# Optimization experiments

Hardware: AMD Instinct MI355X
Metric: run time of the kernel (lower is better)

The kernel has to match this reference:

```python
import jax, jax.numpy as jnp
import numpy as np

E = 8        # n_routed_experts
K = 4        # num_experts_per_tok
T = 1024     # tokens
H = 1024     # hidden_size
I = 1408     # moe_intermediate_size


def setup_inputs() -> dict:
    key = jax.random.key(0)
    ks = jax.random.split(key, 6)
    hidden_states = jax.random.normal(ks[0], (T, H), jnp.float32)
    rw = jax.random.uniform(ks[1], (T, K), jnp.float32)
    router_weights = rw / jnp.sum(rw, axis=-1, keepdims=True)  # normalized top-k router weights
    selected_experts = jax.random.randint(ks[2], (T, K), 0, E, jnp.int32)
    gate_w = jax.random.normal(ks[3], (E, H, I), jnp.float32) * (H ** -0.5)  # lecun_normal-ish
    up_w = jax.random.normal(ks[4], (E, H, I), jnp.float32) * (H ** -0.5)
    down_w = jax.random.normal(ks[5], (E, I, H), jnp.float32) * (I ** -0.5)
    return {
        'hidden_states': hidden_states,
        'router_weights': router_weights,
        'gate_w': gate_w,
        'up_w': up_w,
        'down_w': down_w,
        'selected_experts': selected_experts,
    }


def _grouped_matmul(x, w, seg):
    # x: [m, k] tokens sorted by expert; w: [E, k, n]; seg: [m] expert id per row.
    # Grouped GEMM expressed as E masked GEMMs (fixed small loop over experts);
    # a custom kernel would do true variable-group-size grouped GEMM.
    out = jnp.zeros((x.shape[0], w.shape[-1]), x.dtype)
    for e in range(w.shape[0]):
        out = out + jnp.where((seg == e)[:, None], x, jnp.zeros((), x.dtype)) @ w[e]
    return out


def reference(hidden_states, router_weights, gate_w, up_w, down_w, selected_experts):
    t, k = selected_experts.shape
    flat = selected_experts.ravel()                       # [t*k]
    hs = jnp.repeat(hidden_states, k, axis=0)             # [t*k, H]
    sort_idx = jnp.argsort(flat)                          # dispatch: sort tokens by expert
    seg = flat[sort_idx]
    xs = hs[sort_idx]
    gate = _grouped_matmul(xs, gate_w, seg)               # [t*k, I]
    up = _grouped_matmul(xs, up_w, seg)                   # [t*k, I]
    h = jax.nn.silu(gate) * up                            # fused SwiGLU
    down = _grouped_matmul(h, down_w, seg)                # [t*k, H]
    unsort = jnp.argsort(sort_idx)                        # scatter back to token order
    out = down[unsort].reshape(t, k, -1)
    return jnp.sum(out * router_weights[..., None], axis=1)  # weighted combine [t, H]
```

## Files before the change

### kernel.cpp

```cpp
#include <hip/hip_runtime.h>
#include <hip/hip_bf16.h>
#include <cstdint>
#include <cstddef>

#define NE 8
#define NT 1024
#define NK 4
#define NH 1024
#define NI 1408
#define NA (NT * NK)
#define BM 128
#define MAXTILES 40
#define PADSLOTS 5120

typedef short short8 __attribute__((ext_vector_type(8)));
typedef float f32x4 __attribute__((ext_vector_type(4)));
typedef float f4v __attribute__((ext_vector_type(4)));
typedef unsigned short u16;

#define WS_HDR   0
#define WS_SORT  1024
#define WS_XBF   21504
#define WS_GT    2118656
#define WS_UT    25187328
#define WS_DT    48256000
#define WS_HB    71324672

__device__ __forceinline__ u16 f2b(float f) {
  union { float f; uint32_t u; } c; c.f = f;
  uint32_t u = c.u;
  return (u16)((u + 0x7FFFu + ((u >> 16) & 1u)) >> 16);
}

__device__ __forceinline__ void llds16(const void* g, void* l) {
  __builtin_amdgcn_global_load_lds(
      (const __attribute__((address_space(1))) void*)g,
      (__attribute__((address_space(3))) void*)l, 16, 0, 0);
}

__device__ __forceinline__ void transcvt_stripe(const float* __restrict__ src,
                                                u16* __restrict__ dst,
                                                int K, int N, int k0, int n0,
                                                u16* smem, int tid) {
  u16 (*t2)[64][64] = (u16(*)[64][64])smem;
  int r = tid >> 4, c = tid & 15;
  f4v v[2][4];
#pragma unroll
  for (int t = 0; t < 2; ++t)
#pragma unroll
    for (int i = 0; i < 4; ++i)
      v[t][i] = __builtin_nontemporal_load(
          (const f4v*)&src[(size_t)(k0 + r + 16 * i) * N + n0 + t * 64 + c * 4]);
#pragma unroll
  for (int t = 0; t < 2; ++t)
#pragma unroll
    for (int i = 0; i < 4; ++i) {
      ushort4 o;
      o.x = f2b(v[t][i].x); o.y = f2b(v[t][i].y); o.z = f2b(v[t][i].z); o.w = f2b(v[t][i].w);
      int row = r + 16 * i;
      int sc = (c * 4) ^ (row & 56);
      *(ushort4*)&t2[t][row][sc] = o;
    }
  __syncthreads();
#pragma unroll
  for (int t = 0; t < 2; ++t)
#pragma unroll
    for (int i = 0; i < 2; ++i) {
      int idx = i * 256 + tid;
      int n = idx >> 3, kc = idx & 7;
      int cs = n ^ (kc * 8);
      u16 o[8];
#pragma unroll
      for (int j = 0; j < 8; ++j) o[j] = t2[t][kc * 8 + j][cs];
      *(short8*)&dst[(size_t)(n0 + t * 64 + n) * K + k0 + kc * 8] = *(const short8*)o;
    }
}

__global__ __launch_bounds__(256) void k1_prep(
    const float* __restrict__ gw, const float* __restrict__ uw, const float* __restrict__ dw,
    const float* __restrict__ hs, const int* __restrict__ sel,
    u16* __restrict__ gT, u16* __restrict__ uT, u16* __restrict__ dT, u16* __restrict__ xbf,
    int* __restrict__ hdr, int* __restrict__ sorted, float* __restrict__ outz) {
  int tid = threadIdx.x;
  int y = blockIdx.y;
  if (y == 24) {
    for (int i = blockIdx.x * 256 + tid; i * 4 < NT * NH; i += 176 * 256) {
      f4v v = __builtin_nontemporal_load((const f4v*)&hs[i * 4]);
      ushort4 o;
      o.x = f2b(v.x); o.y = f2b(v.y); o.z = f2b(v.z); o.w = f2b(v.w);
      *(ushort4*)&xbf[i * 4] = o;
    }
    return;
  }
  if (y == 25) {
    int x = blockIdx.x;
    if (x >= 1 && x <= 64) {
      int base = (x - 1) * 16384;
      f4v z = {0.f, 0.f, 0.f, 0.f};
#pragma unroll
      for (int i = 0; i < 16; ++i)
        *(f4v*)&outz[base + (i * 256 + tid) * 4] = z;
      return;
    }
    if (x != 0) return;
    __shared__ int cnt[NE], fill[NE], poff_s[NE + 1];
    if (tid < NE) { cnt[tid] = 0; fill[tid] = 0; }
    __syncthreads();
    for (int i = tid; i < NA; i += 256) atomicAdd(&cnt[sel[i]], 1);
    __syncthreads();
    if (tid == 0) {
      int off = 0, nt = 0;
      for (int e = 0; e < NE; ++e) {
        poff_s[e] = off;
        int tiles = (cnt[e] + BM - 1) / BM;
        for (int j = 0; j < tiles; ++j) { hdr[32 + nt] = e; hdr[80 + nt] = off + j * BM; ++nt; }
        off += tiles * BM;
      }
      poff_s[NE] = off;
      hdr[17] = nt;
      for (int e = 0; e < NE; ++e) hdr[e] = cnt[e];
      for (int e = 0; e <= NE; ++e) hdr[8 + e] = poff_s[e];
    }
    __syncthreads();
    for (int i = tid; i < PADSLOTS; i += 256) sorted[i] = -1;
    __syncthreads();
    for (int i = tid; i < NA; i += 256) {
      int e = sel[i];
      int p = atomicAdd(&fill[e], 1);
      sorted[poff_s[e] + p] = i;
    }
    return;
  }
  __shared__ u16 smem[2 * 64 * 64];
  if (y < 16) {
    int tensor = y >> 3, e = y & 7;
    const float* src = ((tensor == 0) ? gw : uw) + (size_t)e * NH * NI;
    u16* dst = ((tensor == 0) ? gT : uT) + (size_t)e * NH * NI;
    int nb = blockIdx.x % 11, kb = blockIdx.x / 11;
    transcvt_stripe(src, dst, NH, NI, kb * 64, nb * 128, smem, tid);
  } else {
    int e = y - 16;
    const float* src = dw + (size_t)e * NI * NH;
    u16* dst = dT + (size_t)e * NI * NH;
    int nb = blockIdx.x % 8, kb = blockIdx.x / 8;
    transcvt_stripe(src, dst, NI, NH, kb * 64, nb * 128, smem, tid);
  }
}

__global__ __launch_bounds__(256, 2) void k2_gemm1(
    const u16* __restrict__ xbf, const u16* __restrict__ gT, const u16* __restrict__ uT,
    u16* __restrict__ hbuf, const int* __restrict__ hdr, const int* __restrict__ sorted) {
  __shared__ u16 smem[36864];
  int b = blockIdx.x;
  int tid = threadIdx.x;

  int tile = b % 40;
  if (tile >= hdr[17]) return;
  int e = hdr[32 + tile];
  int slot0 = hdr[80 + tile];
  int n0 = (b / 40) * 128;

  const u16* aptr[2];
  const u16 *bgp[2], *bup[2];
#pragma unroll
  for (int s = 0; s < 2; ++s) {
    int idx = s * 256 + tid;
    int row = idx >> 2, c = idx & 3;
    int kc = c ^ (row & 3) ^ ((row >> 2) & 3);
    int as = sorted[slot0 + row];
    int trow = (as >= 0) ? (as >> 2) : 0;
    aptr[s] = xbf + (size_t)trow * NH + kc * 8;
    size_t o = ((size_t)e * NI + n0 + row) * NH + kc * 8;
    bgp[s] = gT + o; bup[s] = uT + o;
  }

  int lane = tid & 63, wave = tid >> 6;
  int wm = wave >> 1, wn = wave & 1;
  int l15 = lane & 15, quad = lane >> 4;
  int pos = ((quad ^ (l15 & 3) ^ ((l15 >> 2) & 3)) & 3) * 8;

  f32x4 accg[4][4] = {}; f32x4 accu[4][4] = {};

#define K2_STAGE(BUF, KT)                                                \
  {                                                                      \
    int ko_ = (KT) * 32;                                                 \
    u16* p_ = smem + (BUF) * 12288;                                      \
    llds16(aptr[0] + ko_, p_ + tid * 8);                                 \
    llds16(aptr[1] + ko_, p_ + (256 + tid) * 8);                         \
    llds16(bgp[0] + ko_, p_ + 4096 + tid * 8);                           \
    llds16(bgp[1] + ko_, p_ + 4096 + (256 + tid) * 8);                   \
    llds16(bup[0] + ko_, p_ + 8192 + tid * 8);                           \
    llds16(bup[1] + ko_, p_ + 8192 + (256 + tid) * 8);                   \
  }

  K2_STAGE(0, 0);
  K2_STAGE(1, 1);
  for (int kt = 0; kt < 32; ++kt) {
    if (kt == 31) { asm volatile("s_waitcnt vmcnt(0)" ::: "memory"); }
    else          { asm volatile("s_waitcnt vmcnt(6)" ::: "memory"); }
    __builtin_amdgcn_s_barrier();
    __builtin_amdgcn_sched_barrier(0);
    if (kt < 30) K2_STAGE((kt + 2) % 3, kt + 2);
    const u16* sA  = smem + (kt % 3) * 12288;
    const u16* sBg = sA + 4096;
    const u16* sBu = sA + 8192;
    short8 av[4], bg[4], bu[4];
#pragma unroll
    for (int mf = 0; mf < 4; ++mf)
      av[mf] = *(const short8*)&sA[(wm * 64 + mf * 16 + l15) * 32 + pos];
#pragma unroll
    for (int nf = 0; nf < 4; ++nf) {
      bg[nf] = *(const short8*)&sBg[(wn * 64 + nf * 16 + l15) * 32 + pos];
      bu[nf] = *(const short8*)&sBu[(wn * 64 + nf * 16 + l15) * 32 + pos];
    }
#pragma unroll
    for (int mf = 0; mf < 4; ++mf)
#pragma unroll
      for (int nf = 0; nf < 4; ++nf) {
        accg[mf][nf] = __builtin_amdgcn_mfma_f32_16x16x32_bf16(av[mf], bg[nf], accg[mf][nf], 0, 0, 0);
        accu[mf][nf] = __builtin_amdgcn_mfma_f32_16x16x32_bf16(av[mf], bu[nf], accu[mf][nf], 0, 0, 0);
      }
  }
#undef K2_STAGE

  for (int mf = 0; mf < 4; ++mf)
    for (int nf = 0; nf < 4; ++nf)
      for (int r = 0; r < 4; ++r) {
        int row = wm * 64 + mf * 16 + quad * 4 + r;
        int col = n0 + wn * 64 + nf * 16 + l15;
        float g2 = accg[mf][nf][r], u = accu[mf][nf][r];
        float hv = (g2 / (1.f + __expf(-g2))) * u;
        hbuf[(size_t)(slot0 + row) * NI + col] = f2b(hv);
      }
}

__global__ __launch_bounds__(256, 3) void k3_gemm2(
    const u16* __restrict__ hbuf, const u16* __restrict__ dT,
    const float* __restrict__ rw, float* __restrict__ out,
    const int* __restrict__ hdr, const int* __restrict__ sorted) {
  __shared__ u16 smem[24576];
  int tile = blockIdx.x;
  if (tile >= hdr[17]) return;
  int e = hdr[32 + tile];
  int slot0 = hdr[80 + tile];
  int n0 = blockIdx.y * 128;
  int tid = threadIdx.x;

  const u16 *ap[2], *bp[2];
#pragma unroll
  for (int s = 0; s < 2; ++s) {
    int idx = s * 256 + tid;
    int row = idx >> 2, c = idx & 3;
    int kc = c ^ (row & 3) ^ ((row >> 2) & 3);
    ap[s] = hbuf + (size_t)(slot0 + row) * NI + kc * 8;
    bp[s] = dT + ((size_t)e * NH + n0 + row) * NI + kc * 8;
  }

  int lane = tid & 63, wave = tid >> 6;
  int wm = wave >> 1, wn = wave & 1;
  int l15 = lane & 15, quad = lane >> 4;
  int pos = ((quad ^ (l15 & 3) ^ ((l15 >> 2) & 3)) & 3) * 8;

  f32x4 acc[4][4] = {};

#define K3_STAGE(BUF, KT)                                                \
  {                                                                      \
    int ko_ = (KT) * 32;                                                 \
    u16* p_ = smem + (BUF) * 8192;                                       \
    llds16(ap[0] + ko_, p_ + tid * 8);                                   \
    llds16(ap[1] + ko_, p_ + (256 + tid) * 8);                           \
    llds16(bp[0] + ko_, p_ + 4096 + tid * 8);                            \
    llds16(bp[1] + ko_, p_ + 4096 + (256 + tid) * 8);                    \
  }

  K3_STAGE(0, 0);
  K3_STAGE(1, 1);
  for (int kt = 0; kt < 44; ++kt) {
    if (kt == 43) { asm volatile("s_waitcnt vmcnt(0)" ::: "memory"); }
    else          { asm volatile("s_waitcnt vmcnt(4)" ::: "memory"); }
    __builtin_amdgcn_s_barrier();
    __builtin_amdgcn_sched_barrier(0);
    if (kt < 42) K3_STAGE((kt + 2) % 3, kt + 2);
    const u16* sA = smem + (kt % 3) * 8192;
    const u16* sB = sA + 4096;
    short8 av[4], bv[4];
#pragma unroll
    for (int mf = 0; mf < 4; ++mf)
      av[mf] = *(const short8*)&sA[(wm * 64 + mf * 16 + l15) * 32 + pos];
#pragma unroll
    for (int nf = 0; nf < 4; ++nf)
      bv[nf] = *(const short8*)&sB[(wn * 64 + nf * 16 + l15) * 32 + pos];
#pragma unroll
    for (int mf = 0; mf < 4; ++mf)
#pragma unroll
      for (int nf = 0; nf < 4; ++nf)
        acc[mf][nf] = __builtin_amdgcn_mfma_f32_16x16x32_bf16(av[mf], bv[nf], acc[mf][nf], 0, 0, 0);
  }
#undef K3_STAGE

  for (int mf = 0; mf < 4; ++mf) {
    int rowb = wm * 64 + mf * 16 + quad * 4;
    for (int r = 0; r < 4; ++r) {
      int as = sorted[slot0 + rowb + r];
      if (as < 0) continue;
      float w = rw[as];
      float* orow = out + (size_t)(as >> 2) * NH + n0 + wn * 64;
      for (int nf = 0; nf < 4; ++nf)
        atomicAdd(&orow[nf * 16 + l15], w * acc[mf][nf][r]);
    }
  }
}

extern "C" void kernel_launch(void* const* d_in, const int* in_sizes, int n_in,
                              void* d_out, int out_size, void* d_ws, size_t ws_size,
                              hipStream_t stream) {
  const float* hs  = (const float*)d_in[0];
  const float* rw  = (const float*)d_in[1];
  const float* gw  = (const float*)d_in[2];
  const float* uw  = (const float*)d_in[3];
  const float* dw  = (const float*)d_in[4];
  const int*   sel = (const int*)d_in[5];
  float* out = (float*)d_out;

  char* ws = (char*)d_ws;
  int*  hdr    = (int*)(ws + WS_HDR);
  int*  sorted = (int*)(ws + WS_SORT);
  u16*  xbf    = (u16*)(ws + WS_XBF);
  u16*  gT     = (u16*)(ws + WS_GT);
  u16*  uT     = (u16*)(ws + WS_UT);
  u16*  dT     = (u16*)(ws + WS_DT);
  u16*  hb     = (u16*)(ws + WS_HB);

  hipLaunchKernelGGL(k1_prep, dim3(176, 26), dim3(256), 0, stream,
                     gw, uw, dw, hs, sel, gT, uT, dT, xbf, hdr, sorted, out);
  hipLaunchKernelGGL(k2_gemm1, dim3(440), dim3(256), 0, stream,
                     xbf, gT, uT, hb, hdr, sorted);
  hipLaunchKernelGGL(k3_gemm2, dim3(MAXTILES, NH / 128), dim3(256), 0, stream,
                     hb, dT, rw, out, hdr, sorted);
}
```

Before: 247.9 us.

## Replace atomic output accumulation with per-slot partials and a combine kernel

The down-projection kernel now writes weighted per-slot partial rows into a scratch buffer that reuses the gate-weight workspace, instead of doing float atomicAdds into the output. A new combine kernel sums the four slot rows for each token through a slot-of map built during dispatch. The prep kernel therefore no longer zeroes the output. Block-to-tile mappings in both GEMM kernels are also remapped, presumably for cache locality across the 8 XCDs. This adds a fourth launch and extra partial-buffer traffic in exchange for removing atomic contention.

Result: faster. 239.4 us (-3.4%).

```diff
diff --git a/kernel.cpp b/kernel.cpp
--- a/kernel.cpp
+++ b/kernel.cpp
@@ -25,6 +25,7 @@
 #define WS_UT    25187328
 #define WS_DT    48256000
 #define WS_HB    71324672
+#define WS_SLOT  (WS_HB + 4992 * NI * 2)
 
 __device__ __forceinline__ u16 f2b(float f) {
   union { float f; uint32_t u; } c; c.f = f;
@@ -80,7 +81,7 @@
     const float* __restrict__ gw, const float* __restrict__ uw, const float* __restrict__ dw,
     const float* __restrict__ hs, const int* __restrict__ sel,
     u16* __restrict__ gT, u16* __restrict__ uT, u16* __restrict__ dT, u16* __restrict__ xbf,
-    int* __restrict__ hdr, int* __restrict__ sorted, float* __restrict__ outz) {
+    int* __restrict__ hdr, int* __restrict__ sorted, int* __restrict__ slotOf) {
   int tid = threadIdx.x;
   int y = blockIdx.y;
   if (y == 24) {
@@ -93,16 +94,7 @@
     return;
   }
   if (y == 25) {
-    int x = blockIdx.x;
-    if (x >= 1 && x <= 64) {
-      int base = (x - 1) * 16384;
-      f4v z = {0.f, 0.f, 0.f, 0.f};
-#pragma unroll
-      for (int i = 0; i < 16; ++i)
-        *(f4v*)&outz[base + (i * 256 + tid) * 4] = z;
-      return;
-    }
-    if (x != 0) return;
+    if (blockIdx.x != 0) return;
     __shared__ int cnt[NE], fill[NE], poff_s[NE + 1];
     if (tid < NE) { cnt[tid] = 0; fill[tid] = 0; }
     __syncthreads();
@@ -127,7 +119,9 @@
     for (int i = tid; i < NA; i += 256) {
       int e = sel[i];
       int p = atomicAdd(&fill[e], 1);
-      sorted[poff_s[e] + p] = i;
+      int s = poff_s[e] + p;
+      sorted[s] = i;
+      slotOf[i] = s;
     }
     return;
   }
@@ -154,11 +148,12 @@
   int b = blockIdx.x;
   int tid = threadIdx.x;
 
-  int tile = b % 40;
+  int job = (b & 7) * 55 + (b >> 3);
+  int tile = job % 40;
   if (tile >= hdr[17]) return;
   int e = hdr[32 + tile];
   int slot0 = hdr[80 + tile];
-  int n0 = (b / 40) * 128;
+  int n0 = (job / 40) * 128;
 
   const u16* aptr[2];
   const u16 *bgp[2], *bup[2];
@@ -236,14 +231,15 @@
 
 __global__ __launch_bounds__(256, 3) void k3_gemm2(
     const u16* __restrict__ hbuf, const u16* __restrict__ dT,
-    const float* __restrict__ rw, float* __restrict__ out,
+    const float* __restrict__ rw, float* __restrict__ part,
     const int* __restrict__ hdr, const int* __restrict__ sorted) {
   __shared__ u16 smem[24576];
-  int tile = blockIdx.x;
+  int b = blockIdx.x;
+  int tile = b >> 3;
   if (tile >= hdr[17]) return;
   int e = hdr[32 + tile];
   int slot0 = hdr[80 + tile];
-  int n0 = blockIdx.y * 128;
+  int n0 = (b & 7) * 128;
   int tid = threadIdx.x;
 
   const u16 *ap[2], *bp[2];
@@ -301,14 +297,34 @@
   for (int mf = 0; mf < 4; ++mf) {
     int rowb = wm * 64 + mf * 16 + quad * 4;
     for (int r = 0; r < 4; ++r) {
-      int as = sorted[slot0 + rowb + r];
+      int slot = slot0 + rowb + r;
+      int as = sorted[slot];
       if (as < 0) continue;
       float w = rw[as];
-      float* orow = out + (size_t)(as >> 2) * NH + n0 + wn * 64;
+      float* prow = part + (size_t)slot * NH + n0 + wn * 64;
       for (int nf = 0; nf < 4; ++nf)
-        atomicAdd(&orow[nf * 16 + l15], w * acc[mf][nf][r]);
-    }
-  }
+        prow[nf * 16 + l15] = w * acc[mf][nf][r];
+    }
+  }
+}
+
+__global__ __launch_bounds__(256) void k4_combine(
+    const float* __restrict__ part, const int* __restrict__ slotOf,
+    float* __restrict__ out) {
+  int tid = threadIdx.x;
+  int token = blockIdx.x * 2 + (tid >> 7);
+  int col0 = (tid & 127) * 8;
+  const int* sl = slotOf + token * 4;
+  f4v a0 = {0.f, 0.f, 0.f, 0.f}, a1 = {0.f, 0.f, 0.f, 0.f};
+#pragma unroll
+  for (int k = 0; k < 4; ++k) {
+    const float* pr = part + (size_t)sl[k] * NH + col0;
+    a0 += *(const f4v*)pr;
+    a1 += *(const f4v*)(pr + 4);
+  }
+  float* o = out + (size_t)token * NH + col0;
+  *(f4v*)o = a0;
+  *(f4v*)(o + 4) = a1;
 }
 
 extern "C" void kernel_launch(void* const* d_in, const int* in_sizes, int n_in,
@@ -330,11 +346,15 @@
   u16*  uT     = (u16*)(ws + WS_UT);
   u16*  dT     = (u16*)(ws + WS_DT);
   u16*  hb     = (u16*)(ws + WS_HB);
+  float* part  = (float*)(ws + WS_GT);
+  int*  slotOf = (int*)(ws + WS_SLOT);
 
   hipLaunchKernelGGL(k1_prep, dim3(176, 26), dim3(256), 0, stream,
-                     gw, uw, dw, hs, sel, gT, uT, dT, xbf, hdr, sorted, out);
+                     gw, uw, dw, hs, sel, gT, uT, dT, xbf, hdr, sorted, slotOf);
   hipLaunchKernelGGL(k2_gemm1, dim3(440), dim3(256), 0, stream,
                      xbf, gT, uT, hb, hdr, sorted);
-  hipLaunchKernelGGL(k3_gemm2, dim3(MAXTILES, NH / 128), dim3(256), 0, stream,
-                     hb, dT, rw, out, hdr, sorted);
-}
+  hipLaunchKernelGGL(k3_gemm2, dim3(320), dim3(256), 0, stream,
+                     hb, dT, rw, part, hdr, sorted);
+  hipLaunchKernelGGL(k4_combine, dim3(512), dim3(256), 0, stream,
+                     part, slotOf, out);
+}
```
